# Performance work log

Measured on AMD Instinct MI355X. Metric: run time of the kernel, lower is better.

## Reference

```python
import jax, jax.numpy as jnp
import numpy as np
from jax import lax

B, T, C, U = 32, 512, 4233, 64


def setup_inputs() -> dict:
    key = jax.random.key(0)
    k1, k2 = jax.random.split(key)
    logits = jax.random.normal(k1, (B, T, C), dtype=jnp.float32)
    ctc_logit = jax.nn.log_softmax(logits, axis=-1)  # [B, T, C] log-probs
    # labels in [1, C) so none equal blank (code treats blank-valued labels as pad)
    label = jax.random.randint(k2, (U, B), 1, C, dtype=jnp.int32)  # [U, B]
    return {"ctc_logit": ctc_logit, "label": label, "blank_id": 0}


def ctc_fa(ctc_logit, label, blank_id):
    pad_value = jnp.finfo(ctc_logit.dtype).min
    lab = label.T  # [B, U]
    lab = jnp.where(lab == blank_id, -1, lab)
    Bb, Uu = lab.shape
    Tt = ctc_logit.shape[1]
    Cc = ctc_logit.shape[2]
    yl = (lab >= 0).sum(1) * 2 + 1  # [B] extended label length
    # interleave blanks: [blank, l0, blank, l1, ..., blank] -> lab_T = 2U+1
    blanks = jnp.full_like(lab, blank_id)
    ext = jnp.stack([blanks, lab], axis=2).reshape(Bb, 2 * Uu)
    ext = jnp.pad(ext, ((0, 0), (0, 1)), constant_values=blank_id)  # [B, labT]
    labT = 2 * Uu + 1
    shifted2 = jnp.pad(ext, ((0, 0), (2, 0)), constant_values=-1)[:, :labT]
    cond = (ext == blank_id) | (ext == shifted2)  # [B, labT]
    ext_idx = ext % Cc  # mimic torch negative-index wrap for -1 pad labels
    # emission log-probs gathered per extended-label position: [B, T, labT]
    emit = jnp.take_along_axis(ctc_logit, ext_idx[:, None, :], axis=2)
    dp0 = jnp.full((Bb, labT), pad_value, ctc_logit.dtype)
    dp0 = dp0.at[:, 0].set(emit[:, 0, 0]).at[:, 1].set(emit[:, 0, 1])
    jrange = jnp.arange(labT)

    def shift(x, n):
        return jnp.pad(x, ((0, 0), (n, 0)), constant_values=pad_value)[:, :labT]

    def step(dp_prev, emit_t):
        s1 = shift(dp_prev, 1)
        s2 = shift(dp_prev, 2)
        a2 = jnp.stack([dp_prev, s1], axis=-1)          # [B, labT, 2]
        a3 = jnp.stack([dp_prev, s1, s2], axis=-1)      # [B, labT, 3]
        idx1 = jnp.argmax(a2, axis=-1)
        idx2 = jnp.argmax(a3, axis=-1)
        lse2 = jax.scipy.special.logsumexp(a2, axis=-1)
        lse3 = jax.scipy.special.logsumexp(a3, axis=-1)
        dp_t = emit_t + jnp.where(cond, lse2, lse3)
        bp_t = jrange[None, :] - jnp.where(cond, idx1, idx2)
        return dp_t, (dp_t, bp_t)

    emit_tbj = jnp.swapaxes(emit, 0, 1)  # [T, B, labT]
    dp_last, (_, bps) = lax.scan(step, dp0, emit_tbj[1:])
    bp0 = jnp.broadcast_to(jrange[None, None, :], (1, Bb, labT)).astype(bps.dtype)
    bp_all = jnp.concatenate([bp0, bps], axis=0)  # [T, B, labT]
    bi = jnp.arange(Bb)
    d1 = dp_last[bi, yl - 1]
    d2 = dp_last[bi, yl - 2]
    ctc_loss = -jnp.logaddexp(d1, d2)
    ctc_loss = 2 * ctc_loss / (yl - 1)
    # Viterbi backtrack -> hard alignment [B, T, labT]
    wi0 = jnp.where(d1 > d2, yl - 1, yl - 2)

    def bstep(wi, bp_t):
        align_t = (jrange[None, :] == wi[:, None]).astype(jnp.int32)
        wi_next = jnp.take_along_axis(bp_t, wi[:, None], axis=1)[:, 0]
        return wi_next, align_t

    _, align_ts = lax.scan(bstep, wi0, bp_all, reverse=True)  # [T, B, labT]
    align = jnp.swapaxes(align_ts, 0, 1)  # [B, T, labT]
    return align, ctc_loss


def reference(ctc_logit, label, blank_id):
    return ctc_fa(ctc_logit, label, blank_id)
```

## Files before the change

kernel.cpp:

```cpp
#include <hip/hip_runtime.h>
#include <math.h>

#define NB 32
#define NT 512
#define NC 4233
#define NU 64
#define LABT 129
#define PADV (-3.4028234663852886e38f)


__device__ __forceinline__ int extcol(int c, const int* label, int b, int blank) {
    if ((c & 1) == 0) return blank;
    int raw = label[((c - 1) >> 1) * NB + b];
    int e = (raw == blank) ? -1 : raw;
    int idx = e % NC;
    if (idx < 0) idx += NC;
    return idx;
}

__device__ __forceinline__ int condcell(int c, const int* label, int b, int blank) {
    if ((c & 1) == 0) return 1;
    int u = (c - 1) >> 1;
    int raw = label[u * NB + b];
    int e = (raw == blank) ? -1 : raw;
    int s2;
    if (u == 0) s2 = -1;
    else {
        int raw2 = label[(u - 1) * NB + b];
        s2 = (raw2 == blank) ? -1 : raw2;
    }
    return (e == blank) || (e == s2);
}

__global__ void ctc_gather_kernel(const float* __restrict__ logit,
                                  const int*   __restrict__ label,
                                  const int*   __restrict__ blank_ptr,
                                  float* __restrict__ emit)
{
    int tid = blockIdx.x * blockDim.x + threadIdx.x;
    int blank = blank_ptr[0];
    int k = tid & 127;
    int bt = tid >> 7;
    int b  = bt >> 9;
    int c  = (k & 1) ? 64 + (k >> 1) : (k >> 1);
    int col = extcol(c, label, b, blank);
    emit[tid] = logit[(size_t)bt * NC + col];
}

__global__ __launch_bounds__(64)
void ctc_scan_kernel(const float* __restrict__ emitb,
                     const int*   __restrict__ label,
                     const int*   __restrict__ blank_ptr,
                     int*   __restrict__ wout,
                     float* __restrict__ loss_out)
{
    __shared__ unsigned long long bpm[NT][4];
    __shared__ unsigned char     bp2s[NT];
    __shared__ float             dpfin[132];
    __shared__ int               wl[NT];

    const int b = blockIdx.x;
    const int l = threadIdx.x;
    const int blank = blank_ptr[0];

    int rawl = label[l * NB + b];
    unsigned long long ylm = __ballot(rawl != blank);
    const int Y = 2 * (int)__popcll(ylm) + 1;

    const int cnd0 = condcell(l,      label, b, blank);
    const int cnd1 = condcell(64 + l, label, b, blank);

    const int lm1 = (l + 63) & 63;
    const int lm2 = (l + 62) & 63;

    const float2* emrow = (const float2*)emitb + (size_t)b * NT * 64 + l;

    float2 e00 = emrow[0];
    float dp0 = (l <= 1) ? e00.x : PADV;
    float dp1 = PADV;
    float dp2 = PADV;

    float2 r0 = emrow[(size_t)1 * 64];
    float2 r1 = emrow[(size_t)2 * 64];
    float2 r2 = emrow[(size_t)3 * 64];
    float2 r3 = emrow[(size_t)4 * 64];
    float2 r4 = emrow[(size_t)5 * 64];
    float2 r5 = emrow[(size_t)6 * 64];
    float2 r6 = emrow[(size_t)7 * 64];
    float2 r7 = emrow[(size_t)8 * 64];

#define STEP(tcur, rr, tload)                                                   \
    do {                                                                         \
        float a0 = dp0, a1 = dp1, a2 = dp2;                                      \
        float q1_0 = __shfl(a0, lm1);                       \
        float q2_0 = __shfl(a0, lm2);                                            \
        float q1_1 = __shfl(a1, lm1);                                            \
        float q2_1 = __shfl(a1, lm2);                                            \
        float s0m1 = (l >= 1) ? q1_0 : PADV;                                     \
        float s0m2 = (l >= 2) ? q2_0 : PADV;                                     \
        float s1m1 = (l == 0) ? q1_0 : q1_1;                 \
        float s1m2 = (l <= 1) ? q2_0 : q2_1;  \
        float c0 = cnd0 ? PADV : s0m2;                                           \
        float c1 = cnd1 ? PADV : s1m2;                                           \
        float m0 = fmaxf(fmaxf(a0, s0m1), c0);                                   \
        float z0 = m0 + __logf(__expf(a0 - m0) + __expf(s0m1 - m0) +             \
                               __expf(c0 - m0));                                 \
        int   d0 = (a0 >= s0m1 && a0 >= c0) ? 0 : ((s0m1 >= c0) ? 1 : 2);        \
        float m1v = fmaxf(fmaxf(a1, s1m1), c1);                                  \
        float z1 = m1v + __logf(__expf(a1 - m1v) + __expf(s1m1 - m1v) +          \
                                __expf(c1 - m1v));                               \
        int   d1 = (a1 >= s1m1 && a1 >= c1) ? 0 : ((s1m1 >= c1) ? 1 : 2);        \
        float m2 = fmaxf(a2, a1);                 \
        float z2 = m2 + __logf(__expf(a2 - m2) + __expf(a1 - m2));               \
        int   d2 = (a2 >= a1) ? 0 : 1;                                           \
        float e2 = __int_as_float(__builtin_amdgcn_readfirstlane(                \
                       __float_as_int(rr.x)));      \
        dp0 = rr.x + z0;                                                         \
        dp1 = rr.y + z1;                                                         \
        dp2 = e2   + z2;                                                         \
        unsigned long long b00 = __ballot(d0 & 1);                               \
        unsigned long long b01 = __ballot(d0 >> 1);                              \
        unsigned long long b10 = __ballot(d1 & 1);                               \
        unsigned long long b11 = __ballot(d1 >> 1);                              \
        if (l == 0) {                                                            \
            bpm[tcur][0] = b00; bpm[tcur][1] = b01;                              \
            bpm[tcur][2] = b10; bpm[tcur][3] = b11;                              \
        }                                                                        \
        if (l == 63) bp2s[tcur] = (unsigned char)d2;                             \
        if ((tload) <= NT - 1) rr = emrow[(size_t)(tload) * 64];                 \
    } while (0)

    int t = 1;
    for (; t + 7 <= NT - 1; t += 8) {
        STEP(t,     r0, t + 8);
        STEP(t + 1, r1, t + 9);
        STEP(t + 2, r2, t + 10);
        STEP(t + 3, r3, t + 11);
        STEP(t + 4, r4, t + 12);
        STEP(t + 5, r5, t + 13);
        STEP(t + 6, r6, t + 14);
        STEP(t + 7, r7, t + 15);
    }
    STEP(t,     r0, NT); t++;
    STEP(t,     r1, NT); t++;
    STEP(t,     r2, NT); t++;
    STEP(t,     r3, NT); t++;
    STEP(t,     r4, NT); t++;
    STEP(t,     r5, NT); t++;
    STEP(t,     r6, NT);
#undef STEP

    dpfin[l] = dp0;
    dpfin[64 + l] = dp1;
    if (l == 63) dpfin[128] = dp2;
    __syncthreads();

    if (l == 0) {
        float d1v = dpfin[Y - 1];
        float d2v = dpfin[Y - 2];
        float mm = fmaxf(d1v, d2v);
        float la = mm + __logf(__expf(d1v - mm) + __expf(d2v - mm));
        loss_out[b] = -la * 2.0f / (float)(Y - 1);

        int w = (d1v > d2v) ? (Y - 1) : (Y - 2);
#pragma unroll 4
        for (int tt = NT - 1; tt >= 1; --tt) {
            wl[tt] = w;
            unsigned long long w0lo = bpm[tt][0], w1lo = bpm[tt][1];
            unsigned long long w0hi = bpm[tt][2], w1hi = bpm[tt][3];
            int dd2 = (int)bp2s[tt];
            unsigned long long m0 = (w < 64) ? w0lo : w0hi;
            unsigned long long m1 = (w < 64) ? w1lo : w1hi;
            int sh = w & 63;
            int dd = (int)((m0 >> sh) & 1ULL) + 2 * (int)((m1 >> sh) & 1ULL);
            if (w == 128) dd = dd2;
            w -= dd;
        }
        wl[0] = w;
    }
    __syncthreads();
    for (int tt = l; tt < NT; tt += 64) wout[b * NT + tt] = wl[tt];
}

__global__ void ctc_align_kernel(const int* __restrict__ w,
                                 float* __restrict__ out)
{
    int tid = blockIdx.x * blockDim.x + threadIdx.x;
    if (tid >= NB * NT * LABT) return;
    int j  = tid % LABT;
    int bt = tid / LABT;
    out[tid] = (j == w[bt]) ? 1.0f : 0.0f;
}

extern "C" void kernel_launch(void* const* d_in, const int* in_sizes, int n_in,
                              void* d_out, int out_size, void* d_ws, size_t ws_size,
                              hipStream_t stream)
{
    const float* logit = (const float*)d_in[0];
    const int*   label = (const int*)d_in[1];
    const int*   blank = (const int*)d_in[2];

    float* out = (float*)d_out;
    int*   ws  = (int*)d_ws;

    int*   wout = ws;
    size_t emit_elems = (size_t)NB * NT * 128;
    bool   use_ws = ws_size >= (size_t)NB * NT * 4 + emit_elems * 4 + 256;
    float* emit = use_ws ? (float*)(ws + NB * NT) : out;

    ctc_gather_kernel<<<(int)(emit_elems / 256), 256, 0, stream>>>(
        logit, label, blank, emit);
    ctc_scan_kernel<<<NB, 64, 0, stream>>>(emit, label, blank, wout,
                                           out + (size_t)NB * NT * LABT);
    int total = NB * NT * LABT;
    ctc_align_kernel<<<(total + 255) / 256, 256, 0, stream>>>(wout, out);
}
```

Baseline: 547.0 us.

## Interleave CTC lattice columns per lane and use DPP shift for recurrence

```diff
diff --git a/kernel.cpp b/kernel.cpp
--- a/kernel.cpp
+++ b/kernel.cpp
@@ -9,18 +9,21 @@
 #define PADV (-3.4028234663852886e38f)
 
 
-__device__ __forceinline__ int extcol(int c, const int* label, int b, int blank) {
-    if ((c & 1) == 0) return blank;
-    int raw = label[((c - 1) >> 1) * NB + b];
+__device__ __forceinline__ float wave_shr1(float x, float fill) {
+    int r = __builtin_amdgcn_update_dpp(__float_as_int(fill), __float_as_int(x),
+                                        0x138, 0xF, 0xF, false);
+    return __int_as_float(r);
+}
+
+__device__ __forceinline__ int oddcol(int u, const int* label, int b, int blank) {
+    int raw = label[u * NB + b];
     int e = (raw == blank) ? -1 : raw;
     int idx = e % NC;
     if (idx < 0) idx += NC;
     return idx;
 }
 
-__device__ __forceinline__ int condcell(int c, const int* label, int b, int blank) {
-    if ((c & 1) == 0) return 1;
-    int u = (c - 1) >> 1;
+__device__ __forceinline__ int oddcond(int u, const int* label, int b, int blank) {
     int raw = label[u * NB + b];
     int e = (raw == blank) ? -1 : raw;
     int s2;
@@ -35,26 +38,28 @@
 __global__ void ctc_gather_kernel(const float* __restrict__ logit,
                                   const int*   __restrict__ label,
                                   const int*   __restrict__ blank_ptr,
-                                  float* __restrict__ emit)
+                                  float* __restrict__ eo,
+                                  float* __restrict__ eb)
 {
     int tid = blockIdx.x * blockDim.x + threadIdx.x;
     int blank = blank_ptr[0];
-    int k = tid & 127;
-    int bt = tid >> 7;
+    int k  = tid & 63;
+    int bt = tid >> 6;
     int b  = bt >> 9;
-    int c  = (k & 1) ? 64 + (k >> 1) : (k >> 1);
-    int col = extcol(c, label, b, blank);
-    emit[tid] = logit[(size_t)bt * NC + col];
+    int col = oddcol(k, label, b, blank);
+    eo[tid] = logit[(size_t)bt * NC + col];
+    if (k == 0) eb[bt] = logit[(size_t)bt * NC + blank];
 }
 
 __global__ __launch_bounds__(64)
-void ctc_scan_kernel(const float* __restrict__ emitb,
+void ctc_scan_kernel(const float* __restrict__ eo,
+                     const float* __restrict__ ebg,
                      const int*   __restrict__ label,
                      const int*   __restrict__ blank_ptr,
                      int*   __restrict__ wout,
                      float* __restrict__ loss_out)
 {
-    __shared__ unsigned long long bpm[NT][4];
+    __shared__ unsigned long long bpm[NT][3];
     __shared__ unsigned char     bp2s[NT];
     __shared__ float             dpfin[132];
     __shared__ int               wl[NT];
@@ -67,92 +72,82 @@
     unsigned long long ylm = __ballot(rawl != blank);
     const int Y = 2 * (int)__popcll(ylm) + 1;
 
-    const int cnd0 = condcell(l,      label, b, blank);
-    const int cnd1 = condcell(64 + l, label, b, blank);
-
-    const int lm1 = (l + 63) & 63;
-    const int lm2 = (l + 62) & 63;
-
-    const float2* emrow = (const float2*)emitb + (size_t)b * NT * 64 + l;
-
-    float2 e00 = emrow[0];
-    float dp0 = (l <= 1) ? e00.x : PADV;
-    float dp1 = PADV;
+    const int cnd1 = oddcond(l, label, b, blank);
+
+    const float* eor = eo  + ((size_t)b * NT) * 64 + l;
+    const float* ebr = ebg + (size_t)b * NT;
+
+    float eb0 = ebr[0];
+    float eo0 = eor[0];
+    float dp0 = (l == 0) ? eb0 : PADV;
+    float dp1 = (l == 0) ? eo0 : PADV;
     float dp2 = PADV;
 
-    float2 r0 = emrow[(size_t)1 * 64];
-    float2 r1 = emrow[(size_t)2 * 64];
-    float2 r2 = emrow[(size_t)3 * 64];
-    float2 r3 = emrow[(size_t)4 * 64];
-    float2 r4 = emrow[(size_t)5 * 64];
-    float2 r5 = emrow[(size_t)6 * 64];
-    float2 r6 = emrow[(size_t)7 * 64];
-    float2 r7 = emrow[(size_t)8 * 64];
-
-#define STEP(tcur, rr, tload)                                                   \
+    float r0 = eor[(size_t)1 * 64], s0 = ebr[1];
+    float r1 = eor[(size_t)2 * 64], s1r = ebr[2];
+    float r2 = eor[(size_t)3 * 64], s2r = ebr[3];
+    float r3 = eor[(size_t)4 * 64], s3r = ebr[4];
+    float r4 = eor[(size_t)5 * 64], s4r = ebr[5];
+    float r5 = eor[(size_t)6 * 64], s5r = ebr[6];
+    float r6 = eor[(size_t)7 * 64], s6r = ebr[7];
+    float r7 = eor[(size_t)8 * 64], s7r = ebr[8];
+
+#define STEP(tcur, rr, sb, tload)                                                \
     do {                                                                         \
         float a0 = dp0, a1 = dp1, a2 = dp2;                                      \
-        float q1_0 = __shfl(a0, lm1);                       \
-        float q2_0 = __shfl(a0, lm2);                                            \
-        float q1_1 = __shfl(a1, lm1);                                            \
-        float q2_1 = __shfl(a1, lm2);                                            \
-        float s0m1 = (l >= 1) ? q1_0 : PADV;                                     \
-        float s0m2 = (l >= 2) ? q2_0 : PADV;                                     \
-        float s1m1 = (l == 0) ? q1_0 : q1_1;                 \
-        float s1m2 = (l <= 1) ? q2_0 : q2_1;  \
-        float c0 = cnd0 ? PADV : s0m2;                                           \
-        float c1 = cnd1 ? PADV : s1m2;                                           \
-        float m0 = fmaxf(fmaxf(a0, s0m1), c0);                                   \
-        float z0 = m0 + __logf(__expf(a0 - m0) + __expf(s0m1 - m0) +             \
-                               __expf(c0 - m0));                                 \
-        int   d0 = (a0 >= s0m1 && a0 >= c0) ? 0 : ((s0m1 >= c0) ? 1 : 2);        \
-        float m1v = fmaxf(fmaxf(a1, s1m1), c1);                                  \
-        float z1 = m1v + __logf(__expf(a1 - m1v) + __expf(s1m1 - m1v) +          \
-                                __expf(c1 - m1v));                               \
-        int   d1 = (a1 >= s1m1 && a1 >= c1) ? 0 : ((s1m1 >= c1) ? 1 : 2);        \
-        float m2 = fmaxf(a2, a1);                 \
-        float z2 = m2 + __logf(__expf(a2 - m2) + __expf(a1 - m2));               \
-        int   d2 = (a2 >= a1) ? 0 : 1;                                           \
-        float e2 = __int_as_float(__builtin_amdgcn_readfirstlane(                \
-                       __float_as_int(rr.x)));      \
-        dp0 = rr.x + z0;                                                         \
-        dp1 = rr.y + z1;                                                         \
-        dp2 = e2   + z2;                                                         \
-        unsigned long long b00 = __ballot(d0 & 1);                               \
-        unsigned long long b01 = __ballot(d0 >> 1);                              \
-        unsigned long long b10 = __ballot(d1 & 1);                               \
-        unsigned long long b11 = __ballot(d1 >> 1);                              \
+        float sp = wave_shr1(a1, PADV);           \
+                              \
+        float m0 = fmaxf(a0, sp);                                                \
+        float z0 = m0 + __logf(__expf(a0 - m0) + __expf(sp - m0));               \
+        unsigned long long bb0 = __ballot(a0 < sp);             \
+                             \
+        float c1 = cnd1 ? PADV : sp;                                             \
+        float m1 = fmaxf(fmaxf(a1, a0), c1);                                     \
+        float z1 = m1 + __logf(__expf(a1 - m1) + __expf(a0 - m1) +               \
+                               __expf(c1 - m1));                                 \
+        int d1 = (a1 >= a0 && a1 >= c1) ? 0 : ((a0 >= c1) ? 1 : 2);              \
+        unsigned long long bb1 = __ballot(d1 & 1);                               \
+        unsigned long long bb2 = __ballot(d1 >> 1);                              \
+               \
+        float s127 = __int_as_float(                                             \
+            __builtin_amdgcn_readlane(__float_as_int(a1), 63));                  \
+        float m2 = fmaxf(a2, s127);                                              \
+        float z2 = m2 + __logf(__expf(a2 - m2) + __expf(s127 - m2));             \
+        int d2u = (a2 >= s127) ? 0 : 1;                                          \
+        dp0 = sb + z0;                                                           \
+        dp1 = rr + z1;                                                           \
+        dp2 = sb + z2;                                                           \
         if (l == 0) {                                                            \
-            bpm[tcur][0] = b00; bpm[tcur][1] = b01;                              \
-            bpm[tcur][2] = b10; bpm[tcur][3] = b11;                              \
+            bpm[tcur][0] = bb0; bpm[tcur][1] = bb1; bpm[tcur][2] = bb2;          \
+            bp2s[tcur] = (unsigned char)d2u;                                     \
         }                                                                        \
-        if (l == 63) bp2s[tcur] = (unsigned char)d2;                             \
-        if ((tload) <= NT - 1) rr = emrow[(size_t)(tload) * 64];                 \
+        if ((tload) <= NT - 1) { rr = eor[(size_t)(tload) * 64];                 \
+                                 sb = ebr[tload]; }                              \
     } while (0)
 
     int t = 1;
     for (; t + 7 <= NT - 1; t += 8) {
-        STEP(t,     r0, t + 8);
-        STEP(t + 1, r1, t + 9);
-        STEP(t + 2, r2, t + 10);
-        STEP(t + 3, r3, t + 11);
-        STEP(t + 4, r4, t + 12);
-        STEP(t + 5, r5, t + 13);
-        STEP(t + 6, r6, t + 14);
-        STEP(t + 7, r7, t + 15);
-    }
-    STEP(t,     r0, NT); t++;
-    STEP(t,     r1, NT); t++;
-    STEP(t,     r2, NT); t++;
-    STEP(t,     r3, NT); t++;
-    STEP(t,     r4, NT); t++;
-    STEP(t,     r5, NT); t++;
-    STEP(t,     r6, NT);
+        STEP(t,     r0, s0,  t + 8);
+        STEP(t + 1, r1, s1r, t + 9);
+        STEP(t + 2, r2, s2r, t + 10);
+        STEP(t + 3, r3, s3r, t + 11);
+        STEP(t + 4, r4, s4r, t + 12);
+        STEP(t + 5, r5, s5r, t + 13);
+        STEP(t + 6, r6, s6r, t + 14);
+        STEP(t + 7, r7, s7r, t + 15);
+    }
+    STEP(t,     r0, s0,  NT); t++;
+    STEP(t,     r1, s1r, NT); t++;
+    STEP(t,     r2, s2r, NT); t++;
+    STEP(t,     r3, s3r, NT); t++;
+    STEP(t,     r4, s4r, NT); t++;
+    STEP(t,     r5, s5r, NT); t++;
+    STEP(t,     r6, s6r, NT);
 #undef STEP
 
-    dpfin[l] = dp0;
-    dpfin[64 + l] = dp1;
-    if (l == 63) dpfin[128] = dp2;
+    dpfin[2 * l]     = dp0;
+    dpfin[2 * l + 1] = dp1;
+    if (l == 0) dpfin[128] = dp2;
     __syncthreads();
 
     if (l == 0) {
@@ -166,14 +161,15 @@
 #pragma unroll 4
         for (int tt = NT - 1; tt >= 1; --tt) {
             wl[tt] = w;
-            unsigned long long w0lo = bpm[tt][0], w1lo = bpm[tt][1];
-            unsigned long long w0hi = bpm[tt][2], w1hi = bpm[tt][3];
-            int dd2 = (int)bp2s[tt];
-            unsigned long long m0 = (w < 64) ? w0lo : w0hi;
-            unsigned long long m1 = (w < 64) ? w1lo : w1hi;
-            int sh = w & 63;
-            int dd = (int)((m0 >> sh) & 1ULL) + 2 * (int)((m1 >> sh) & 1ULL);
-            if (w == 128) dd = dd2;
+            unsigned long long B0 = bpm[tt][0];
+            unsigned long long B1 = bpm[tt][1];
+            unsigned long long B2 = bpm[tt][2];
+            int d2v2 = (int)bp2s[tt];
+            int li = w >> 1;
+            int dd;
+            if (w == 128)     dd = d2v2;
+            else if (w & 1)   dd = (int)((B1 >> li) & 1ULL) + 2 * (int)((B2 >> li) & 1ULL);
+            else              dd = (int)((B0 >> li) & 1ULL);
             w -= dd;
         }
         wl[0] = w;
@@ -204,13 +200,22 @@
     int*   ws  = (int*)d_ws;
 
     int*   wout = ws;
-    size_t emit_elems = (size_t)NB * NT * 128;
-    bool   use_ws = ws_size >= (size_t)NB * NT * 4 + emit_elems * 4 + 256;
-    float* emit = use_ws ? (float*)(ws + NB * NT) : out;
-
-    ctc_gather_kernel<<<(int)(emit_elems / 256), 256, 0, stream>>>(
-        logit, label, blank, emit);
-    ctc_scan_kernel<<<NB, 64, 0, stream>>>(emit, label, blank, wout,
+    size_t need = (size_t)NB * NT * 4
+                + (size_t)NB * NT * 4
+                + (size_t)NB * NT * 64 * 4 + 256;
+    bool   use_ws = ws_size >= need;
+    float* ebp, *eop;
+    if (use_ws) {
+        ebp = (float*)(ws + NB * NT);
+        eop = ebp + NB * NT;
+    } else {
+        ebp = out;
+        eop = out + NB * NT;
+    }
+
+    ctc_gather_kernel<<<NB * NT * 64 / 256, 256, 0, stream>>>(
+        logit, label, blank, eop, ebp);
+    ctc_scan_kernel<<<NB, 64, 0, stream>>>(eop, ebp, label, blank, wout,
                                            out + (size_t)NB * NT * LABT);
     int total = NB * NT * LABT;
     ctc_align_kernel<<<(total + 255) / 256, 256, 0, stream>>>(wout, out);
```

Result: faster. 533.1 us (-2.5%).
